# Optimization experiments

Measured on AMD Instinct MI355X. Metric: run time of the kernel, lower is better.

The kernel has to match this reference:

```python
import jax, jax.numpy as jnp
import numpy as np

HEAD_DIM = 64

def setup_inputs() -> dict:
    key = jax.random.key(0)
    k1, k2, k3, k4, k5 = jax.random.split(key, 5)
    T, B, E = 2048, 4, 1024
    KD = 64  # kdim
    x = jax.random.normal(k1, (T, B, E), dtype=jnp.float32)
    in_proj_weight = jax.random.normal(k2, (3 * KD, HEAD_DIM), dtype=jnp.float32) * (1.0 / np.sqrt(HEAD_DIM))
    in_proj_bias = jnp.zeros((3 * KD,), dtype=jnp.float32)
    out_w = jax.random.normal(k4, (HEAD_DIM, KD), dtype=jnp.float32) * (1.0 / np.sqrt(KD))
    out_b = jnp.zeros((HEAD_DIM,), dtype=jnp.float32)
    return {"x": x, "in_proj_weight": in_proj_weight, "in_proj_bias": in_proj_bias,
            "out_w": out_w, "out_b": out_b}

def reference(x, in_proj_weight, in_proj_bias, out_w, out_b):
    # x: [T, B, E] with E = H * HEAD_DIM (qkv_same self-attention path)
    T, B, E = x.shape
    H = E // HEAD_DIM
    KD = in_proj_weight.shape[0] // 3
    scaling = HEAD_DIM ** (-0.5)
    # reshape splits embed dim into heads: [T, B*H, 64]
    xh = x.reshape(T, B * H, HEAD_DIM)
    # fused in-projection: [T, B*H, 3*KD], then chunk into q/k/v
    qkv = xh @ in_proj_weight.T + in_proj_bias
    q, k, v = jnp.split(qkv, 3, axis=-1)          # each [T, B*H, KD]
    q = q * scaling
    q = q.transpose(1, 0, 2)                      # [B*H, T, KD]
    k = k.transpose(1, 0, 2)
    v = v.transpose(1, 0, 2)
    scores = jnp.einsum('btd,bsd->bts', q, k)     # [B*H, T, T]
    w = jax.nn.softmax(scores, axis=-1)
    attn = jnp.einsum('bts,bsd->btd', w, v)       # [B*H, T, KD]
    attn = attn.transpose(1, 0, 2).reshape(T, B, H, KD)
    out = attn @ out_w.T + out_b                  # [T, B, H, HEAD_DIM]
    out = out.reshape(T, B, H * HEAD_DIM)         # [T, B, E]
    # averaged attention weights over heads: [B, T, T]
    avg_w = w.reshape(B, H, T, T).sum(axis=1) / H
    return out, avg_w
```

## Files before the change

kernel.cpp:

```cpp
#include <hip/hip_runtime.h>
#include <hip/hip_bf16.h>

#define T_DIM 2048
#define B_DIM 4
#define E_DIM 1024

typedef __bf16 bf16_t;
typedef bf16_t bf16x8 __attribute__((ext_vector_type(8)));
typedef float f32x4 __attribute__((ext_vector_type(4)));
typedef float f32x16 __attribute__((ext_vector_type(16)));

union frag_u { uint4 u; bf16x8 b; };

constexpr float SCALEQ = 0.18033688011112042f;

__device__ __forceinline__ f32x16 mfma32(bf16x8 a, bf16x8 b, f32x16 c) {
  return __builtin_amdgcn_mfma_f32_32x32x16_bf16(a, b, c, 0, 0, 0);
}
__device__ __forceinline__ unsigned packbf(float a, float b) {
  union { bf16_t h[2]; unsigned u; } r;
  r.h[0] = (bf16_t)a; r.h[1] = (bf16_t)b; return r.u;
}
__device__ __forceinline__ void pl32swap(unsigned &x, unsigned &y) {
  asm volatile("v_permlane32_swap_b32 %0, %1" : "+v"(x), "+v"(y));
}
__device__ __forceinline__ void gload16(const void* g, void* l) {
  __builtin_amdgcn_global_load_lds((const __attribute__((address_space(1))) void*)g,
                                   (__attribute__((address_space(3))) void*)l, 16, 0, 0);
}
__device__ __forceinline__ bf16x8 ldc(const char* base, int chunk, int row) {
  frag_u f; f.u = *(const uint4*)(base + chunk * 1024 + row * 16); return f.b;
}
__device__ __forceinline__ float ex2(float x) { return __builtin_amdgcn_exp2f(x); }

#define VMCNT4 do { asm volatile("s_waitcnt vmcnt(4)" ::: "memory"); \
                    __builtin_amdgcn_sched_barrier(0); } while (0)
#define VMCNT0 do { asm volatile("s_waitcnt vmcnt(0)" ::: "memory"); \
                    __builtin_amdgcn_sched_barrier(0); } while (0)
#define LGKM0  do { asm volatile("s_waitcnt lgkmcnt(0)" ::: "memory"); \
                    __builtin_amdgcn_sched_barrier(0); } while (0)
#define SBAR   do { __builtin_amdgcn_s_barrier(); \
                    __builtin_amdgcn_sched_barrier(0); } while (0)

template <int O>
__device__ __forceinline__ uint4 mkfrag(const f32x16& A) {
  unsigned X = packbf(A[O + 0], A[O + 1]);
  unsigned Z = packbf(A[O + 2], A[O + 3]);
  unsigned Y = packbf(A[O + 4], A[O + 5]);
  unsigned W = packbf(A[O + 6], A[O + 7]);
  pl32swap(X, Y); pl32swap(Z, W);
  return (uint4){X, Z, Y, W};
}

__global__ __launch_bounds__(256) void qkv_kernel(
    const float* __restrict__ x, const float* __restrict__ W,
    const float* __restrict__ bias,
    bf16_t* __restrict__ Qc, bf16_t* __restrict__ Kc, bf16_t* __restrict__ Vc) {
  __shared__ __align__(16) char xlds[16384];
  __shared__ __align__(16) char wlds[24576];
  __shared__ float bs[192];
  const int tid = threadIdx.x;
  const int bh = blockIdx.x >> 4;
  const int tt = blockIdx.x & 15;
  const int b = bh >> 4, h = bh & 15;
  const int t0 = tt * 128;
  const int wid = tid >> 6, lane = tid & 63;
  const int lq = lane & 31, hi = lane >> 5;

  for (int i = tid; i < 1024; i += 256) {
    int t = i >> 3, oct = i & 7;
    const float* src = x + ((size_t)(t0 + t) * B_DIM + b) * E_DIM + h * 64 + oct * 8;
    float4 f0 = *(const float4*)src;
    float4 f1 = *(const float4*)(src + 4);
    uint4 u;
    u.x = packbf(f0.x, f0.y); u.y = packbf(f0.z, f0.w);
    u.z = packbf(f1.x, f1.y); u.w = packbf(f1.z, f1.w);
    *(uint4*)(xlds + oct * 2048 + t * 16) = u;
  }
  for (int i = tid; i < 1536; i += 256) {
    int r = i >> 3, oct = i & 7;
    const float* src = W + r * 64 + oct * 8;
    float4 f0 = *(const float4*)src;
    float4 f1 = *(const float4*)(src + 4);
    uint4 u;
    u.x = packbf(f0.x, f0.y); u.y = packbf(f0.z, f0.w);
    u.z = packbf(f1.x, f1.y); u.w = packbf(f1.z, f1.w);
    *(uint4*)(wlds + oct * 3072 + r * 16) = u;
  }
  if (tid < 192) bs[tid] = bias[tid];
  __syncthreads();

  frag_u bx[4];
  #pragma unroll
  for (int s = 0; s < 4; ++s)
    bx[s].u = *(const uint4*)(xlds + (s * 2 + hi) * 2048 + (wid * 32 + lq) * 16);

  f32x16 acc[6];
  #pragma unroll
  for (int mt = 0; mt < 6; ++mt)
    #pragma unroll
    for (int r = 0; r < 16; ++r) acc[mt][r] = 0.f;

  #pragma unroll
  for (int mt = 0; mt < 6; ++mt) {
    #pragma unroll
    for (int s = 0; s < 4; ++s) {
      frag_u aw;
      aw.u = *(const uint4*)(wlds + (s * 2 + hi) * 3072 + (mt * 32 + lq) * 16);
      acc[mt] = mfma32(aw.b, bx[s].b, acc[mt]);
    }
  }

  const size_t tb = ((size_t)bh * 32 + (t0 >> 6) + (wid >> 1)) * 4096;
  const int trow = (wid & 1) * 32 + lq;

  #pragma unroll
  for (int mt = 0; mt < 6; ++mt) {
    #pragma unroll
    for (int g = 0; g < 4; ++g) {
      int rbase = mt * 32 + 8 * g + 4 * hi;
      float4 bq = *(const float4*)&bs[rbase];
      float v0 = acc[mt][4 * g + 0] + bq.x;
      float v1 = acc[mt][4 * g + 1] + bq.y;
      float v2 = acc[mt][4 * g + 2] + bq.z;
      float v3 = acc[mt][4 * g + 3] + bq.w;
      if (mt < 2) {
        union { ushort4 us; unsigned u2[2]; } pk;
        pk.u2[0] = packbf(v0 * SCALEQ, v1 * SCALEQ);
        pk.u2[1] = packbf(v2 * SCALEQ, v3 * SCALEQ);
        int d0 = rbase;
        *(ushort4*)(Qc + tb + (d0 >> 3) * 512 + trow * 8 + (d0 & 7)) = pk.us;
      } else if (mt < 4) {
        union { ushort4 us; unsigned u2[2]; } pk;
        pk.u2[0] = packbf(v0, v1);
        pk.u2[1] = packbf(v2, v3);
        int d0 = rbase - 64;
        *(ushort4*)(Kc + tb + (d0 >> 3) * 512 + trow * 8 + (d0 & 7)) = pk.us;
      } else {
        int d0 = rbase - 128;
        bf16_t* vdst = Vc + tb + (trow >> 3) * 512 + (trow & 7);
        vdst[(size_t)(d0 + 0) * 8] = (bf16_t)v0;
        vdst[(size_t)(d0 + 1) * 8] = (bf16_t)v1;
        vdst[(size_t)(d0 + 2) * 8] = (bf16_t)v2;
        vdst[(size_t)(d0 + 3) * 8] = (bf16_t)v3;
      }
    }
  }
}

__global__ __launch_bounds__(256, 2) void flash_kernel(
    const bf16_t* __restrict__ Qc, const bf16_t* __restrict__ Kc,
    const bf16_t* __restrict__ Vc,
    const float* __restrict__ Wo, const float* __restrict__ bo,
    float* __restrict__ out, float* __restrict__ Lv) {
  __shared__ __align__(16) char lds[32768];
  __shared__ __align__(16) char wlds[8192];
  const int tid = threadIdx.x;
  const int bid = ((blockIdx.x & 7) << 6) | (blockIdx.x >> 3);
  const int bh = bid >> 3, qb = bid & 7;
  const int b = bh >> 4, h = bh & 15;
  const int wid = tid >> 6, lane = tid & 63;
  const int lq = lane & 31, hi = lane >> 5;
  const int qw = qb * 256 + wid * 64;

  for (int i = tid; i < 512; i += 256) {
    int d = i >> 3, oct = i & 7;
    const float* src = Wo + d * 64 + oct * 8;
    float4 f0 = *(const float4*)src;
    float4 f1 = *(const float4*)(src + 4);
    uint4 u;
    u.x = packbf(f0.x, f0.y); u.y = packbf(f0.z, f0.w);
    u.z = packbf(f1.x, f1.y); u.w = packbf(f1.z, f1.w);
    *(uint4*)(wlds + oct * 1024 + d * 16) = u;
  }

  const bf16_t* qtb = Qc + ((size_t)bh * 32 + (qw >> 6)) * 4096;
  frag_u qfA[4], qfB[4];
  #pragma unroll
  for (int s = 0; s < 4; ++s) {
    qfA[s].u = *(const uint4*)(qtb + (s * 2 + hi) * 512 + lq * 8);
    qfB[s].u = *(const uint4*)(qtb + (s * 2 + hi) * 512 + (32 + lq) * 8);
  }

  f32x16 zc;
  #pragma unroll
  for (int i = 0; i < 16; ++i) zc[i] = 0.f;

  f32x16 oA0, oA1, oB0, oB1;
  #pragma unroll
  for (int i = 0; i < 16; ++i) { oA0[i] = 0.f; oA1[i] = 0.f; oB0[i] = 0.f; oB1[i] = 0.f; }
  float lAacc = 0.f, lBacc = 0.f;

  const bf16_t* kbh = Kc + (size_t)bh * 131072;
  const bf16_t* vbh = Vc + (size_t)bh * 131072;
  auto stage = [&](int buf, int t) {
    char* kl_ = lds + buf * 16384 + wid * 1024;
    char* vl_ = kl_ + 8192;
    const bf16_t* kt = kbh + (size_t)t * 4096 + wid * 512 + lane * 8;
    const bf16_t* vt = vbh + (size_t)t * 4096 + wid * 512 + lane * 8;
    gload16(kt, kl_); gload16(kt + 2048, kl_ + 4096);
    gload16(vt, vl_); gload16(vt + 2048, vl_ + 4096);
  };

  stage(0, 0); stage(1, 1);
  VMCNT4; LGKM0;
  SBAR;

  bf16x8 k0[4], k1[4];
  {
    const char* kl = lds;
    #pragma unroll
    for (int s = 0; s < 4; ++s) {
      k0[s] = ldc(kl, s * 2 + hi, lq);
      k1[s] = ldc(kl, s * 2 + hi, 32 + lq);
    }
  }
  f32x16 aA0, aA1;
  aA0 = mfma32(k0[0], qfA[0].b, zc);
  aA1 = mfma32(k1[0], qfA[0].b, zc);
  #pragma unroll
  for (int s = 1; s < 4; ++s) {
    aA0 = mfma32(k0[s], qfA[s].b, aA0);
    aA1 = mfma32(k1[s], qfA[s].b, aA1);
  }

  for (int t = 0; t < 32; ++t) {
    const char* cb = lds + (t & 1) * 16384;
    const char* vl = cb + 8192;

    f32x16 aB0, aB1;
    __builtin_amdgcn_s_setprio(1);
    aB0 = mfma32(k0[0], qfB[0].b, zc);
    aB1 = mfma32(k1[0], qfB[0].b, zc);
    #pragma unroll
    for (int s = 1; s < 4; ++s) {
      aB0 = mfma32(k0[s], qfB[s].b, aB0);
      aB1 = mfma32(k1[s], qfB[s].b, aB1);
    }
    __builtin_amdgcn_s_setprio(0);
    float sA = 0.f;
    #pragma unroll
    for (int i = 0; i < 16; ++i) {
      aA0[i] = ex2(aA0[i]); sA += aA0[i];
      aA1[i] = ex2(aA1[i]); sA += aA1[i];
    }
    lAacc += sA;
    frag_u pA0, pA1, pA2, pA3;
    pA0.u = mkfrag<0>(aA0); pA1.u = mkfrag<8>(aA0);
    pA2.u = mkfrag<0>(aA1); pA3.u = mkfrag<8>(aA1);

    bf16x8 v0[4], v1[4];
    #pragma unroll
    for (int ks = 0; ks < 4; ++ks) {
      v0[ks] = ldc(vl, ks * 2 + hi, lq);
      v1[ks] = ldc(vl, ks * 2 + hi, 32 + lq);
    }

    __builtin_amdgcn_s_setprio(1);
    oA0 = mfma32(v0[0], pA0.b, oA0); oA1 = mfma32(v1[0], pA0.b, oA1);
    oA0 = mfma32(v0[1], pA1.b, oA0); oA1 = mfma32(v1[1], pA1.b, oA1);
    oA0 = mfma32(v0[2], pA2.b, oA0); oA1 = mfma32(v1[2], pA2.b, oA1);
    oA0 = mfma32(v0[3], pA3.b, oA0); oA1 = mfma32(v1[3], pA3.b, oA1);
    __builtin_amdgcn_s_setprio(0);
    float sB = 0.f;
    #pragma unroll
    for (int i = 0; i < 16; ++i) {
      aB0[i] = ex2(aB0[i]); sB += aB0[i];
      aB1[i] = ex2(aB1[i]); sB += aB1[i];
    }
    lBacc += sB;
    frag_u pB0, pB1, pB2, pB3;
    pB0.u = mkfrag<0>(aB0); pB1.u = mkfrag<8>(aB0);
    pB2.u = mkfrag<0>(aB1); pB3.u = mkfrag<8>(aB1);

    VMCNT0;
    SBAR;
    if (t + 2 < 32) stage(t & 1, t + 2);

    __builtin_amdgcn_s_setprio(1);
    oB0 = mfma32(v0[0], pB0.b, oB0); oB1 = mfma32(v1[0], pB0.b, oB1);
    oB0 = mfma32(v0[1], pB1.b, oB0); oB1 = mfma32(v1[1], pB1.b, oB1);
    oB0 = mfma32(v0[2], pB2.b, oB0); oB1 = mfma32(v1[2], pB2.b, oB1);
    oB0 = mfma32(v0[3], pB3.b, oB0); oB1 = mfma32(v1[3], pB3.b, oB1);
    __builtin_amdgcn_s_setprio(0);
    if (t < 31) {
      const char* kn = lds + ((t + 1) & 1) * 16384;
      #pragma unroll
      for (int s = 0; s < 4; ++s) {
        k0[s] = ldc(kn, s * 2 + hi, lq);
        k1[s] = ldc(kn, s * 2 + hi, 32 + lq);
      }
      __builtin_amdgcn_s_setprio(1);
      aA0 = mfma32(k0[0], qfA[0].b, zc);
      aA1 = mfma32(k1[0], qfA[0].b, zc);
      #pragma unroll
      for (int s = 1; s < 4; ++s) {
        aA0 = mfma32(k0[s], qfA[s].b, aA0);
        aA1 = mfma32(k1[s], qfA[s].b, aA1);
      }
      __builtin_amdgcn_s_setprio(0);
    }
  }

  float ltA = lAacc + __shfl_xor(lAacc, 32);
  float ltB = lBacc + __shfl_xor(lBacc, 32);
  float iA = 1.f / ltA, iB = 1.f / ltB;
  #pragma unroll
  for (int i = 0; i < 16; ++i) { oA0[i] *= iA; oA1[i] *= iA; oB0[i] *= iB; oB1[i] *= iB; }

  frag_u fA[4], fB[4];
  fA[0].u = mkfrag<0>(oA0); fA[1].u = mkfrag<8>(oA0);
  fA[2].u = mkfrag<0>(oA1); fA[3].u = mkfrag<8>(oA1);
  fB[0].u = mkfrag<0>(oB0); fB[1].u = mkfrag<8>(oB0);
  fB[2].u = mkfrag<0>(oB1); fB[3].u = mkfrag<8>(oB1);

  f32x16 cA0, cA1, cB0, cB1;
  #pragma unroll
  for (int i = 0; i < 16; ++i) { cA0[i] = 0.f; cA1[i] = 0.f; cB0[i] = 0.f; cB1[i] = 0.f; }
  #pragma unroll
  for (int s = 0; s < 4; ++s) {
    frag_u w0, w1;
    w0.u = *(const uint4*)(wlds + (s * 2 + hi) * 1024 + lq * 16);
    w1.u = *(const uint4*)(wlds + (s * 2 + hi) * 1024 + (32 + lq) * 16);
    cA0 = mfma32(fA[s].b, w0.b, cA0);
    cA1 = mfma32(fA[s].b, w1.b, cA1);
    cB0 = mfma32(fB[s].b, w0.b, cB0);
    cB1 = mfma32(fB[s].b, w1.b, cB1);
  }
  float bo0 = bo[lq], bo1 = bo[32 + lq];
  #pragma unroll
  for (int r = 0; r < 16; ++r) {
    int trA = qw + (r & 3) + 8 * (r >> 2) + 4 * hi;
    int trB = trA + 32;
    out[((size_t)trA * B_DIM + b) * E_DIM + h * 64 + lq]      = cA0[r] + bo0;
    out[((size_t)trA * B_DIM + b) * E_DIM + h * 64 + 32 + lq] = cA1[r] + bo1;
    out[((size_t)trB * B_DIM + b) * E_DIM + h * 64 + lq]      = cB0[r] + bo0;
    out[((size_t)trB * B_DIM + b) * E_DIM + h * 64 + 32 + lq] = cB1[r] + bo1;
  }
  if (lane < 32) {
    Lv[(size_t)bh * T_DIM + qw + lq] = ltA;
    Lv[(size_t)bh * T_DIM + qw + 32 + lq] = ltB;
  }
}

__global__ __launch_bounds__(512, 2) void avgw_kernel(
    const bf16_t* __restrict__ Qc, const bf16_t* __restrict__ Kc,
    const float* __restrict__ Lv, float* __restrict__ avgw) {
  __shared__ __align__(16) char qlds[2][16384];
  __shared__ __align__(16) char klds[2][16384];
  __shared__ float lw[16][128];
  const int tid = threadIdx.x;
  const int bid = ((blockIdx.x & 7) << 7) | (blockIdx.x >> 3);
  const int b = bid >> 8, tq = (bid >> 4) & 15, sq = bid & 15;
  const int t0 = tq * 128, s0 = sq * 128;
  const int wid = tid >> 6, lane = tid & 63;
  const int lq = lane & 31, hi = lane >> 5;
  const int wr = wid >> 2, wc = wid & 3;

  for (int i = tid; i < 2048; i += 512) {
    int h = i >> 7, tt = i & 127;
    size_t idx = ((size_t)(b * 16 + h)) * T_DIM + t0 + tt;
    lw[h][tt] = 1.0f / (16.0f * Lv[idx]);
  }

  auto stage = [&](int buf, int h) {
    int bh = b * 16 + h;
    const bf16_t* qt = Qc + ((size_t)bh * 32 + (t0 >> 6)) * 4096;
    const bf16_t* kt = Kc + ((size_t)bh * 32 + (s0 >> 6)) * 4096;
    #pragma unroll
    for (int j = 0; j < 2; ++j) {
      gload16(qt + wid * 1024 + j * 512 + lane * 8, qlds[buf] + wid * 2048 + j * 1024);
      gload16(kt + wid * 1024 + j * 512 + lane * 8, klds[buf] + wid * 2048 + j * 1024);
    }
  };

  f32x16 zc;
  #pragma unroll
  for (int r = 0; r < 16; ++r) zc[r] = 0.f;

  f32x16 sacc[2];
  #pragma unroll
  for (int i = 0; i < 2; ++i)
    #pragma unroll
    for (int r = 0; r < 16; ++r) sacc[i][r] = 0.f;

  stage(0, 0);
  __syncthreads();

  for (int h = 0; h < 16; ++h) {
    if (h < 15) stage((h + 1) & 1, h + 1);
    const char* qb = qlds[h & 1];
    const char* kb = klds[h & 1];

    frag_u aq[2][4], ak[4];
    #pragma unroll
    for (int s = 0; s < 4; ++s) {
      int rk = wc * 32 + lq;
      ak[s].u = *(const uint4*)(kb + (rk >> 6) * 8192 + (s * 2 + hi) * 1024 + (rk & 63) * 16);
      #pragma unroll
      for (int i = 0; i < 2; ++i) {
        int rq = wr * 64 + i * 32 + lq;
        aq[i][s].u = *(const uint4*)(qb + (rq >> 6) * 8192 + (s * 2 + hi) * 1024 + (rq & 63) * 16);
      }
    }

    #pragma unroll
    for (int i = 0; i < 2; ++i) {
      __builtin_amdgcn_s_setprio(1);
      f32x16 c = mfma32(aq[i][0].b, ak[0].b, zc);
      #pragma unroll
      for (int s = 1; s < 4; ++s) c = mfma32(aq[i][s].b, ak[s].b, c);
      __builtin_amdgcn_s_setprio(0);
      #pragma unroll
      for (int g = 0; g < 4; ++g) {
        f32x4 l4 = *(const f32x4*)&lw[h][wr * 64 + i * 32 + 8 * g + 4 * hi];
        #pragma unroll
        for (int e = 0; e < 4; ++e)
          sacc[i][4 * g + e] += ex2(c[4 * g + e]) * l4[e];
      }
    }
    __syncthreads();
  }

  #pragma unroll
  for (int i = 0; i < 2; ++i)
    #pragma unroll
    for (int r = 0; r < 16; ++r) {
      int trow = t0 + wr * 64 + i * 32 + (r & 3) + ((r >> 2) << 3) + (hi << 2);
      int scol = s0 + wc * 32 + lq;
      avgw[((size_t)b * T_DIM + trow) * T_DIM + scol] = sacc[i][r];
    }
}

extern "C" void kernel_launch(void* const* d_in, const int* in_sizes, int n_in,
                              void* d_out, int out_size, void* d_ws, size_t ws_size,
                              hipStream_t stream) {
  const float* x    = (const float*)d_in[0];
  const float* W    = (const float*)d_in[1];
  const float* bias = (const float*)d_in[2];
  const float* Wo   = (const float*)d_in[3];
  const float* bo   = (const float*)d_in[4];
  float* out  = (float*)d_out;
  float* avgw = out + (size_t)T_DIM * B_DIM * E_DIM;

  char* ws = (char*)d_ws;
  bf16_t* Qc = (bf16_t*)(ws);
  bf16_t* Kc = (bf16_t*)(ws + (16u << 20));
  bf16_t* Vc = (bf16_t*)(ws + (32u << 20));
  float*  Lv = (float*)(ws + (48u << 20));

  qkv_kernel<<<dim3(1024), dim3(256), 0, stream>>>(x, W, bias, Qc, Kc, Vc);
  flash_kernel<<<dim3(512), dim3(256), 0, stream>>>(Qc, Kc, Vc, Wo, bo, out, Lv);
  avgw_kernel<<<dim3(1024), dim3(512), 0, stream>>>(Qc, Kc, Lv, avgw);
}
```

Before: 174.3 us.

## Deepen K/V staging to four-slot ring and load Q fragments directly from global

The flash kernel moves from a two-buffer K/V pipeline with software-skewed QK^T across iterations to a four-slot LDS ring with three tiles in flight, relaxed vmcnt waits, and a simpler per-iteration schedule that computes both A and B score tiles together. The avgw kernel likewise stages only K through a four-slot ring, drops the trailing __syncthreads, and reads Q fragments straight from global memory instead of staging them in LDS. The goal is to hide more global-load latency and cut barrier stalls. In exchange, LDS use per block doubles, which may lower occupancy. Removing the cross-iteration skew also reduces MFMA/exp overlap.

After: 186.9 us. +7.2%, slower.

```diff
diff --git a/kernel.cpp b/kernel.cpp
--- a/kernel.cpp
+++ b/kernel.cpp
@@ -33,7 +33,11 @@
 }
 __device__ __forceinline__ float ex2(float x) { return __builtin_amdgcn_exp2f(x); }
 
+#define VMCNT8 do { asm volatile("s_waitcnt vmcnt(8)" ::: "memory"); \
+                    __builtin_amdgcn_sched_barrier(0); } while (0)
 #define VMCNT4 do { asm volatile("s_waitcnt vmcnt(4)" ::: "memory"); \
+                    __builtin_amdgcn_sched_barrier(0); } while (0)
+#define VMCNT2 do { asm volatile("s_waitcnt vmcnt(2)" ::: "memory"); \
                     __builtin_amdgcn_sched_barrier(0); } while (0)
 #define VMCNT0 do { asm volatile("s_waitcnt vmcnt(0)" ::: "memory"); \
                     __builtin_amdgcn_sched_barrier(0); } while (0)
@@ -153,7 +157,7 @@
     const bf16_t* __restrict__ Vc,
     const float* __restrict__ Wo, const float* __restrict__ bo,
     float* __restrict__ out, float* __restrict__ Lv) {
-  __shared__ __align__(16) char lds[32768];
+  __shared__ __align__(16) char lds[65536];
   __shared__ __align__(16) char wlds[8192];
   const int tid = threadIdx.x;
   const int bid = ((blockIdx.x & 7) << 6) | (blockIdx.x >> 3);
@@ -193,113 +197,81 @@
 
   const bf16_t* kbh = Kc + (size_t)bh * 131072;
   const bf16_t* vbh = Vc + (size_t)bh * 131072;
-  auto stage = [&](int buf, int t) {
-    char* kl_ = lds + buf * 16384 + wid * 1024;
-    char* vl_ = kl_ + 8192;
-    const bf16_t* kt = kbh + (size_t)t * 4096 + wid * 512 + lane * 8;
-    const bf16_t* vt = vbh + (size_t)t * 4096 + wid * 512 + lane * 8;
-    gload16(kt, kl_); gload16(kt + 2048, kl_ + 4096);
-    gload16(vt, vl_); gload16(vt + 2048, vl_ + 4096);
+  auto stage = [&](int slot, int t) {
+    char* kd = lds + slot * 16384;
+    const bf16_t* kt = kbh + (size_t)t * 4096 + tid * 8;
+    const bf16_t* vt = vbh + (size_t)t * 4096 + tid * 8;
+    gload16(kt, kd + tid * 16);
+    gload16(kt + 2048, kd + 4096 + tid * 16);
+    gload16(vt, kd + 8192 + tid * 16);
+    gload16(vt + 2048, kd + 12288 + tid * 16);
   };
 
-  stage(0, 0); stage(1, 1);
-  VMCNT4; LGKM0;
-  SBAR;
-
-  bf16x8 k0[4], k1[4];
-  {
-    const char* kl = lds;
+  stage(0, 0); stage(1, 1); stage(2, 2);
+  LGKM0;
+
+  for (int t = 0; t < 32; ++t) {
+    if (t < 30) { VMCNT8; } else if (t == 30) { VMCNT4; } else { VMCNT0; }
+    SBAR;
+    if (t + 3 < 32) stage((t + 3) & 3, t + 3);
+
+    const char* kl = lds + (t & 3) * 16384;
+    const char* vl = kl + 8192;
+
+    bf16x8 k0[4], k1[4];
     #pragma unroll
     for (int s = 0; s < 4; ++s) {
       k0[s] = ldc(kl, s * 2 + hi, lq);
       k1[s] = ldc(kl, s * 2 + hi, 32 + lq);
     }
-  }
-  f32x16 aA0, aA1;
-  aA0 = mfma32(k0[0], qfA[0].b, zc);
-  aA1 = mfma32(k1[0], qfA[0].b, zc);
-  #pragma unroll
-  for (int s = 1; s < 4; ++s) {
-    aA0 = mfma32(k0[s], qfA[s].b, aA0);
-    aA1 = mfma32(k1[s], qfA[s].b, aA1);
-  }
-
-  for (int t = 0; t < 32; ++t) {
-    const char* cb = lds + (t & 1) * 16384;
-    const char* vl = cb + 8192;
-
-    f32x16 aB0, aB1;
+    f32x16 aA0, aA1, aB0, aB1;
     __builtin_amdgcn_s_setprio(1);
+    aA0 = mfma32(k0[0], qfA[0].b, zc);
+    aA1 = mfma32(k1[0], qfA[0].b, zc);
     aB0 = mfma32(k0[0], qfB[0].b, zc);
     aB1 = mfma32(k1[0], qfB[0].b, zc);
     #pragma unroll
     for (int s = 1; s < 4; ++s) {
+      aA0 = mfma32(k0[s], qfA[s].b, aA0);
+      aA1 = mfma32(k1[s], qfA[s].b, aA1);
       aB0 = mfma32(k0[s], qfB[s].b, aB0);
       aB1 = mfma32(k1[s], qfB[s].b, aB1);
     }
     __builtin_amdgcn_s_setprio(0);
-    float sA = 0.f;
+
+    bf16x8 v0[4], v1[4];
+    #pragma unroll
+    for (int ks = 0; ks < 4; ++ks) {
+      v0[ks] = ldc(vl, ks * 2 + hi, lq);
+      v1[ks] = ldc(vl, ks * 2 + hi, 32 + lq);
+    }
+
+    float sA = 0.f, sB = 0.f;
     #pragma unroll
     for (int i = 0; i < 16; ++i) {
       aA0[i] = ex2(aA0[i]); sA += aA0[i];
       aA1[i] = ex2(aA1[i]); sA += aA1[i];
-    }
-    lAacc += sA;
-    frag_u pA0, pA1, pA2, pA3;
+      aB0[i] = ex2(aB0[i]); sB += aB0[i];
+      aB1[i] = ex2(aB1[i]); sB += aB1[i];
+    }
+    lAacc += sA; lBacc += sB;
+
+    frag_u pA0, pA1, pA2, pA3, pB0, pB1, pB2, pB3;
     pA0.u = mkfrag<0>(aA0); pA1.u = mkfrag<8>(aA0);
     pA2.u = mkfrag<0>(aA1); pA3.u = mkfrag<8>(aA1);
-
-    bf16x8 v0[4], v1[4];
-    #pragma unroll
-    for (int ks = 0; ks < 4; ++ks) {
-      v0[ks] = ldc(vl, ks * 2 + hi, lq);
-      v1[ks] = ldc(vl, ks * 2 + hi, 32 + lq);
-    }
+    pB0.u = mkfrag<0>(aB0); pB1.u = mkfrag<8>(aB0);
+    pB2.u = mkfrag<0>(aB1); pB3.u = mkfrag<8>(aB1);
 
     __builtin_amdgcn_s_setprio(1);
     oA0 = mfma32(v0[0], pA0.b, oA0); oA1 = mfma32(v1[0], pA0.b, oA1);
+    oB0 = mfma32(v0[0], pB0.b, oB0); oB1 = mfma32(v1[0], pB0.b, oB1);
     oA0 = mfma32(v0[1], pA1.b, oA0); oA1 = mfma32(v1[1], pA1.b, oA1);
+    oB0 = mfma32(v0[1], pB1.b, oB0); oB1 = mfma32(v1[1], pB1.b, oB1);
     oA0 = mfma32(v0[2], pA2.b, oA0); oA1 = mfma32(v1[2], pA2.b, oA1);
+    oB0 = mfma32(v0[2], pB2.b, oB0); oB1 = mfma32(v1[2], pB2.b, oB1);
     oA0 = mfma32(v0[3], pA3.b, oA0); oA1 = mfma32(v1[3], pA3.b, oA1);
-    __builtin_amdgcn_s_setprio(0);
-    float sB = 0.f;
-    #pragma unroll
-    for (int i = 0; i < 16; ++i) {
-      aB0[i] = ex2(aB0[i]); sB += aB0[i];
-      aB1[i] = ex2(aB1[i]); sB += aB1[i];
-    }
-    lBacc += sB;
-    frag_u pB0, pB1, pB2, pB3;
-    pB0.u = mkfrag<0>(aB0); pB1.u = mkfrag<8>(aB0);
-    pB2.u = mkfrag<0>(aB1); pB3.u = mkfrag<8>(aB1);
-
-    VMCNT0;
-    SBAR;
-    if (t + 2 < 32) stage(t & 1, t + 2);
-
-    __builtin_amdgcn_s_setprio(1);
-    oB0 = mfma32(v0[0], pB0.b, oB0); oB1 = mfma32(v1[0], pB0.b, oB1);
-    oB0 = mfma32(v0[1], pB1.b, oB0); oB1 = mfma32(v1[1], pB1.b, oB1);
-    oB0 = mfma32(v0[2], pB2.b, oB0); oB1 = mfma32(v1[2], pB2.b, oB1);
     oB0 = mfma32(v0[3], pB3.b, oB0); oB1 = mfma32(v1[3], pB3.b, oB1);
     __builtin_amdgcn_s_setprio(0);
-    if (t < 31) {
-      const char* kn = lds + ((t + 1) & 1) * 16384;
-      #pragma unroll
-      for (int s = 0; s < 4; ++s) {
-        k0[s] = ldc(kn, s * 2 + hi, lq);
-        k1[s] = ldc(kn, s * 2 + hi, 32 + lq);
-      }
-      __builtin_amdgcn_s_setprio(1);
-      aA0 = mfma32(k0[0], qfA[0].b, zc);
-      aA1 = mfma32(k1[0], qfA[0].b, zc);
-      #pragma unroll
-      for (int s = 1; s < 4; ++s) {
-        aA0 = mfma32(k0[s], qfA[s].b, aA0);
-        aA1 = mfma32(k1[s], qfA[s].b, aA1);
-      }
-      __builtin_amdgcn_s_setprio(0);
-    }
   }
 
   float ltA = lAacc + __shfl_xor(lAacc, 32);
@@ -346,8 +318,7 @@
 __global__ __launch_bounds__(512, 2) void avgw_kernel(
     const bf16_t* __restrict__ Qc, const bf16_t* __restrict__ Kc,
     const float* __restrict__ Lv, float* __restrict__ avgw) {
-  __shared__ __align__(16) char qlds[2][16384];
-  __shared__ __align__(16) char klds[2][16384];
+  __shared__ __align__(16) char klds[65536];
   __shared__ float lw[16][128];
   const int tid = threadIdx.x;
   const int bid = ((blockIdx.x & 7) << 7) | (blockIdx.x >> 3);
@@ -363,15 +334,12 @@
     lw[h][tt] = 1.0f / (16.0f * Lv[idx]);
   }
 
-  auto stage = [&](int buf, int h) {
-    int bh = b * 16 + h;
-    const bf16_t* qt = Qc + ((size_t)bh * 32 + (t0 >> 6)) * 4096;
-    const bf16_t* kt = Kc + ((size_t)bh * 32 + (s0 >> 6)) * 4096;
-    #pragma unroll
-    for (int j = 0; j < 2; ++j) {
-      gload16(qt + wid * 1024 + j * 512 + lane * 8, qlds[buf] + wid * 2048 + j * 1024);
-      gload16(kt + wid * 1024 + j * 512 + lane * 8, klds[buf] + wid * 2048 + j * 1024);
-    }
+  const size_t kbase = ((size_t)b * 16) * 131072 + (size_t)(s0 >> 6) * 4096;
+  auto stage = [&](int slot, int h) {
+    const bf16_t* kt = Kc + kbase + (size_t)h * 131072 + tid * 8;
+    char* kd = klds + slot * 16384;
+    gload16(kt, kd + tid * 16);
+    gload16(kt + 4096, kd + 8192 + tid * 16);
   };
 
   f32x16 zc;
@@ -384,23 +352,28 @@
     #pragma unroll
     for (int r = 0; r < 16; ++r) sacc[i][r] = 0.f;
 
-  stage(0, 0);
-  __syncthreads();
+  stage(0, 0); stage(1, 1); stage(2, 2);
+  LGKM0;
+
+  const bf16_t* qbase = Qc + ((size_t)(b * 16)) * 131072 + (size_t)(t0 >> 6) * 4096;
+  const int rk = wc * 32 + lq;
 
   for (int h = 0; h < 16; ++h) {
-    if (h < 15) stage((h + 1) & 1, h + 1);
-    const char* qb = qlds[h & 1];
-    const char* kb = klds[h & 1];
+    if (h < 14) { VMCNT4; } else if (h == 14) { VMCNT2; } else { VMCNT0; }
+    SBAR;
+    if (h + 3 < 16) stage((h + 3) & 3, h + 3);
+
+    const char* kb = klds + (h & 3) * 16384;
+    const bf16_t* qh = qbase + (size_t)h * 131072;
 
     frag_u aq[2][4], ak[4];
     #pragma unroll
     for (int s = 0; s < 4; ++s) {
-      int rk = wc * 32 + lq;
       ak[s].u = *(const uint4*)(kb + (rk >> 6) * 8192 + (s * 2 + hi) * 1024 + (rk & 63) * 16);
       #pragma unroll
       for (int i = 0; i < 2; ++i) {
         int rq = wr * 64 + i * 32 + lq;
-        aq[i][s].u = *(const uint4*)(qb + (rq >> 6) * 8192 + (s * 2 + hi) * 1024 + (rq & 63) * 16);
+        aq[i][s].u = *(const uint4*)(qh + (size_t)(rq >> 6) * 4096 + (s * 2 + hi) * 512 + (rq & 63) * 8);
       }
     }
 
@@ -419,7 +392,6 @@
           sacc[i][4 * g + e] += ex2(c[4 * g + e]) * l4[e];
       }
     }
-    __syncthreads();
   }
 
   #pragma unroll
```

## Restructure attention loop and compute softmax row sums with ones-vector MFMA

Applied to the files above, without the earlier changes.

Replaces the software-pipelined loop, which overlapped the next tile's QK^T with the current PV, with a simpler per-iteration schedule. Each iteration loads K, computes all four score blocks, loads V, then issues the refill of the freed buffer after a barrier. The scalar row-sum accumulation of exponentials is replaced by extra MFMAs against a vector of ones, moving the reduction work from VALU to the matrix unit. Sums are now taken over bf16-rounded probabilities, and the cross-iteration overlap between MFMA and exp work is lost.

Measured after the change: 168.6 us. 3.3% less time.

```diff
diff --git a/kernel.cpp b/kernel.cpp
--- a/kernel.cpp
+++ b/kernel.cpp
@@ -182,14 +182,20 @@
     qfB[s].u = *(const uint4*)(qtb + (s * 2 + hi) * 512 + (32 + lq) * 8);
   }
 
+  frag_u ones;
+  #pragma unroll
+  for (int j = 0; j < 8; ++j) ones.b[j] = (bf16_t)1.0f;
+
   f32x16 zc;
   #pragma unroll
   for (int i = 0; i < 16; ++i) zc[i] = 0.f;
 
-  f32x16 oA0, oA1, oB0, oB1;
-  #pragma unroll
-  for (int i = 0; i < 16; ++i) { oA0[i] = 0.f; oA1[i] = 0.f; oB0[i] = 0.f; oB1[i] = 0.f; }
-  float lAacc = 0.f, lBacc = 0.f;
+  f32x16 oA0, oA1, oB0, oB1, lmfA, lmfB;
+  #pragma unroll
+  for (int i = 0; i < 16; ++i) {
+    oA0[i] = 0.f; oA1[i] = 0.f; oB0[i] = 0.f; oB1[i] = 0.f;
+    lmfA[i] = 0.f; lmfB[i] = 0.f;
+  }
 
   const bf16_t* kbh = Kc + (size_t)bh * 131072;
   const bf16_t* vbh = Vc + (size_t)bh * 131072;
@@ -206,48 +212,30 @@
   VMCNT4; LGKM0;
   SBAR;
 
-  bf16x8 k0[4], k1[4];
-  {
-    const char* kl = lds;
+  for (int t = 0; t < 32; ++t) {
+    const char* kl = lds + (t & 1) * 16384;
+    const char* vl = kl + 8192;
+
+    bf16x8 k0[4], k1[4];
     #pragma unroll
     for (int s = 0; s < 4; ++s) {
       k0[s] = ldc(kl, s * 2 + hi, lq);
       k1[s] = ldc(kl, s * 2 + hi, 32 + lq);
     }
-  }
-  f32x16 aA0, aA1;
-  aA0 = mfma32(k0[0], qfA[0].b, zc);
-  aA1 = mfma32(k1[0], qfA[0].b, zc);
-  #pragma unroll
-  for (int s = 1; s < 4; ++s) {
-    aA0 = mfma32(k0[s], qfA[s].b, aA0);
-    aA1 = mfma32(k1[s], qfA[s].b, aA1);
-  }
-
-  for (int t = 0; t < 32; ++t) {
-    const char* cb = lds + (t & 1) * 16384;
-    const char* vl = cb + 8192;
-
-    f32x16 aB0, aB1;
+    f32x16 aA0, aA1, aB0, aB1;
     __builtin_amdgcn_s_setprio(1);
+    aA0 = mfma32(k0[0], qfA[0].b, zc);
+    aA1 = mfma32(k1[0], qfA[0].b, zc);
     aB0 = mfma32(k0[0], qfB[0].b, zc);
     aB1 = mfma32(k1[0], qfB[0].b, zc);
     #pragma unroll
     for (int s = 1; s < 4; ++s) {
+      aA0 = mfma32(k0[s], qfA[s].b, aA0);
+      aA1 = mfma32(k1[s], qfA[s].b, aA1);
       aB0 = mfma32(k0[s], qfB[s].b, aB0);
       aB1 = mfma32(k1[s], qfB[s].b, aB1);
     }
     __builtin_amdgcn_s_setprio(0);
-    float sA = 0.f;
-    #pragma unroll
-    for (int i = 0; i < 16; ++i) {
-      aA0[i] = ex2(aA0[i]); sA += aA0[i];
-      aA1[i] = ex2(aA1[i]); sA += aA1[i];
-    }
-    lAacc += sA;
-    frag_u pA0, pA1, pA2, pA3;
-    pA0.u = mkfrag<0>(aA0); pA1.u = mkfrag<8>(aA0);
-    pA2.u = mkfrag<0>(aA1); pA3.u = mkfrag<8>(aA1);
 
     bf16x8 v0[4], v1[4];
     #pragma unroll
@@ -255,55 +243,42 @@
       v0[ks] = ldc(vl, ks * 2 + hi, lq);
       v1[ks] = ldc(vl, ks * 2 + hi, 32 + lq);
     }
+    LGKM0;
+    SBAR;
+    if (t + 2 < 32) stage(t & 1, t + 2);
+
+    #pragma unroll
+    for (int i = 0; i < 16; ++i) {
+      aA0[i] = ex2(aA0[i]); aA1[i] = ex2(aA1[i]);
+      aB0[i] = ex2(aB0[i]); aB1[i] = ex2(aB1[i]);
+    }
+
+    frag_u pA0, pA1, pA2, pA3, pB0, pB1, pB2, pB3;
+    pA0.u = mkfrag<0>(aA0); pA1.u = mkfrag<8>(aA0);
+    pA2.u = mkfrag<0>(aA1); pA3.u = mkfrag<8>(aA1);
+    pB0.u = mkfrag<0>(aB0); pB1.u = mkfrag<8>(aB0);
+    pB2.u = mkfrag<0>(aB1); pB3.u = mkfrag<8>(aB1);
 
     __builtin_amdgcn_s_setprio(1);
     oA0 = mfma32(v0[0], pA0.b, oA0); oA1 = mfma32(v1[0], pA0.b, oA1);
+    oB0 = mfma32(v0[0], pB0.b, oB0); oB1 = mfma32(v1[0], pB0.b, oB1);
     oA0 = mfma32(v0[1], pA1.b, oA0); oA1 = mfma32(v1[1], pA1.b, oA1);
+    oB0 = mfma32(v0[1], pB1.b, oB0); oB1 = mfma32(v1[1], pB1.b, oB1);
     oA0 = mfma32(v0[2], pA2.b, oA0); oA1 = mfma32(v1[2], pA2.b, oA1);
+    oB0 = mfma32(v0[2], pB2.b, oB0); oB1 = mfma32(v1[2], pB2.b, oB1);
     oA0 = mfma32(v0[3], pA3.b, oA0); oA1 = mfma32(v1[3], pA3.b, oA1);
+    oB0 = mfma32(v0[3], pB3.b, oB0); oB1 = mfma32(v1[3], pB3.b, oB1);
+    lmfA = mfma32(ones.b, pA0.b, lmfA); lmfA = mfma32(ones.b, pA1.b, lmfA);
+    lmfA = mfma32(ones.b, pA2.b, lmfA); lmfA = mfma32(ones.b, pA3.b, lmfA);
+    lmfB = mfma32(ones.b, pB0.b, lmfB); lmfB = mfma32(ones.b, pB1.b, lmfB);
+    lmfB = mfma32(ones.b, pB2.b, lmfB); lmfB = mfma32(ones.b, pB3.b, lmfB);
     __builtin_amdgcn_s_setprio(0);
-    float sB = 0.f;
-    #pragma unroll
-    for (int i = 0; i < 16; ++i) {
-      aB0[i] = ex2(aB0[i]); sB += aB0[i];
-      aB1[i] = ex2(aB1[i]); sB += aB1[i];
-    }
-    lBacc += sB;
-    frag_u pB0, pB1, pB2, pB3;
-    pB0.u = mkfrag<0>(aB0); pB1.u = mkfrag<8>(aB0);
-    pB2.u = mkfrag<0>(aB1); pB3.u = mkfrag<8>(aB1);
-
-    VMCNT0;
+
+    if (t < 30) { VMCNT4; } else { VMCNT0; }
     SBAR;
-    if (t + 2 < 32) stage(t & 1, t + 2);
-
-    __builtin_amdgcn_s_setprio(1);
-    oB0 = mfma32(v0[0], pB0.b, oB0); oB1 = mfma32(v1[0], pB0.b, oB1);
-    oB0 = mfma32(v0[1], pB1.b, oB0); oB1 = mfma32(v1[1], pB1.b, oB1);
-    oB0 = mfma32(v0[2], pB2.b, oB0); oB1 = mfma32(v1[2], pB2.b, oB1);
-    oB0 = mfma32(v0[3], pB3.b, oB0); oB1 = mfma32(v1[3], pB3.b, oB1);
-    __builtin_amdgcn_s_setprio(0);
-    if (t < 31) {
-      const char* kn = lds + ((t + 1) & 1) * 16384;
-      #pragma unroll
-      for (int s = 0; s < 4; ++s) {
-        k0[s] = ldc(kn, s * 2 + hi, lq);
-        k1[s] = ldc(kn, s * 2 + hi, 32 + lq);
-      }
-      __builtin_amdgcn_s_setprio(1);
-      aA0 = mfma32(k0[0], qfA[0].b, zc);
-      aA1 = mfma32(k1[0], qfA[0].b, zc);
-      #pragma unroll
-      for (int s = 1; s < 4; ++s) {
-        aA0 = mfma32(k0[s], qfA[s].b, aA0);
-        aA1 = mfma32(k1[s], qfA[s].b, aA1);
-      }
-      __builtin_amdgcn_s_setprio(0);
-    }
-  }
-
-  float ltA = lAacc + __shfl_xor(lAacc, 32);
-  float ltB = lBacc + __shfl_xor(lBacc, 32);
+  }
+
+  float ltA = lmfA[0], ltB = lmfB[0];
   float iA = 1.f / ltA, iB = 1.f / ltB;
   #pragma unroll
   for (int i = 0; i < 16; ++i) { oA0[i] *= iA; oA1[i] *= iA; oB0[i] *= iB; oB1[i] *= iB; }
```
